# Optimization experiments

Hardware: AMD Instinct MI355X
Metric: run time of the kernel (lower is better)

Reference implementation:

```python
import jax, jax.numpy as jnp
import numpy as np

HEADS = 4
DIM_QK = 128
SCALE = DIM_QK ** (-0.5)


def rel_to_abs(x):
    # x: [B, Nh, L, 2L-1] -> [B, Nh, L, L] via the skew trick
    B, Nh, L, _ = x.shape
    x = jnp.pad(x, ((0, 0), (0, 0), (0, 0), (0, 1)))          # [B,Nh,L,2L]
    flat = x.reshape(B, Nh, L * 2 * L)
    flat = jnp.pad(flat, ((0, 0), (0, 0), (0, L - 1)))
    final = flat.reshape(B, Nh, L + 1, 2 * L - 1)
    return final[:, :, :L, L - 1:]


def relative_logits_1d(q, rel_k):
    # q: [B, Nh, H, W, d], rel_k: [2W-1, d] -> [B, Nh, H, H, W, W] (axes b h x i y j)
    B, Nh, H, W, _ = q.shape
    rl = jnp.einsum('bnhwd,md->bnhwm', q, rel_k)              # [B,Nh,H,W,2W-1]
    rl = rl.reshape(B, Nh * H, W, 2 * W - 1)
    rl = rel_to_abs(rl)                                        # [B,Nh*H,W,W]
    rl = rl.reshape(B, Nh, H, W, W)
    rl = jnp.broadcast_to(rl[:, :, :, None, :, :], (B, Nh, H, H, W, W))
    return rl


def rel_pos_logits(q, rel_height, rel_width, H, W):
    # q: [B, h, HW, d]
    B, h, L, d = q.shape
    qg = q.reshape(B, h, H, W, d)
    # width direction: b h x i y j -> b h (x y) (i j)
    rw = relative_logits_1d(qg, rel_width)                     # [B,h,H,H,W,W]
    rw = rw.transpose(0, 1, 2, 4, 3, 5).reshape(B, h, H * W, H * W)
    # height direction: transpose x<->y, then b h x i y j -> b h (y x) (j i)
    qh = qg.transpose(0, 1, 3, 2, 4)                           # [B,h,W,H,d]
    rh = relative_logits_1d(qh, rel_height)                    # [B,h,W,W,H,H]
    rh = rh.transpose(0, 1, 4, 2, 5, 3).reshape(B, h, H * W, H * W)
    return rw + rh


def setup_inputs() -> dict:
    key = jax.random.key(0)
    ks = jax.random.split(key, 5)
    B, C, H, W = 16, 512, 32, 32
    scale = DIM_QK ** (-0.5)
    return {
        'featuremap': jax.random.normal(ks[0], (B, C, H, W), jnp.float32),
        'w_qk': jax.random.normal(ks[1], (2 * HEADS * DIM_QK, C), jnp.float32) * (C ** -0.5),
        'w_v': jax.random.normal(ks[2], (HEADS * 128, C), jnp.float32) * (C ** -0.5),
        'rel_height': jax.random.normal(ks[3], (2 * H - 1, DIM_QK), jnp.float32) * scale,
        'rel_width': jax.random.normal(ks[4], (2 * W - 1, DIM_QK), jnp.float32) * scale,
    }


def reference(featuremap, w_qk, w_v, rel_height, rel_width):
    B, C, H, W = featuremap.shape
    L = H * W
    # 1x1 conv projections (no bias) == channel matmuls
    qk = jnp.einsum('bchw,oc->bohw', featuremap, w_qk)         # [B, 2*h*dqk, H, W]
    v = jnp.einsum('bchw,oc->bohw', featuremap, w_v)           # [B, h*dv, H, W]
    q, k = jnp.split(qk, 2, axis=1)

    def to_heads(x):
        # B (h d) H W -> B h (H W) d
        d = x.shape[1] // HEADS
        return x.reshape(B, HEADS, d, L).transpose(0, 1, 3, 2)

    q, k, v = to_heads(q), to_heads(k), to_heads(v)
    q = q * SCALE
    logits = jnp.einsum('bhxd,bhyd->bhxy', q, k)
    logits = logits + rel_pos_logits(q, rel_height, rel_width, H, W)
    weights = jax.nn.softmax(logits, axis=-1)
    attn_out = jnp.einsum('bhxy,bhyd->bhxd', weights, v)       # [B,h,L,dv]
    dv = attn_out.shape[-1]
    # B h (H W) d -> B (h d) H W
    return attn_out.transpose(0, 1, 3, 2).reshape(B, HEADS * dv, H, W)
```

## Files before the change

kernel.cpp:

```cpp
#include <hip/hip_runtime.h>
#include <stdint.h>

typedef __attribute__((ext_vector_type(4))) float f32x4;
typedef __attribute__((ext_vector_type(8))) short bf16x8;

#define DEV static __device__ __forceinline__

#define GLOAD16(g, l) __builtin_amdgcn_global_load_lds( \
    (const __attribute__((address_space(1))) void*)(g), \
    (__attribute__((address_space(3))) void*)(l), 16, 0, 0)

DEV unsigned short f2bf(float f){
  union { float f; uint32_t u; } v; v.f = f;
  return (unsigned short)((v.u + 0x7fffu + ((v.u >> 16) & 1u)) >> 16);
}

DEV uint32_t cvtpk(float a, float b){
  uint32_t r; asm("v_cvt_pk_bf16_f32 %0, %1, %2" : "=v"(r) : "v"(a), "v"(b)); return r;
}

DEV f32x4 mfma_bf16(bf16x8 a, bf16x8 b, f32x4 c){
  return __builtin_amdgcn_mfma_f32_16x16x32_bf16(a, b, c, 0, 0, 0);
}

__global__ __launch_bounds__(256) void k_transpose_cvt(const float* __restrict__ fm,
                                                       unsigned short* __restrict__ xt){
  __shared__ float tile[64][65];
  int b = blockIdx.z, c0 = blockIdx.y * 64, l0 = blockIdx.x * 64;
  int t = threadIdx.x;
  int lr = t >> 4;
  int lc4 = (t & 15) * 4;
  const float* src = fm + ((size_t)b * 512 + c0) * 1024 + l0;
  #pragma unroll
  for (int i = 0; i < 4; i++){
    int r = lr + i * 16;
    f32x4 v = *(const f32x4*)&src[(size_t)r * 1024 + lc4];
    tile[r][lc4] = v[0]; tile[r][lc4 + 1] = v[1];
    tile[r][lc4 + 2] = v[2]; tile[r][lc4 + 3] = v[3];
  }
  __syncthreads();
  int j = t & 7;
  int lrow = t >> 3;
  unsigned short* dst = xt + ((size_t)b * 1024 + l0) * 512 + c0;
  #pragma unroll
  for (int i = 0; i < 2; i++){
    int l = lrow + i * 32;
    unsigned short tmp[8];
    #pragma unroll
    for (int u = 0; u < 8; u++) tmp[u] = f2bf(tile[j * 8 + u][l]);
    *(uint4*)&dst[(size_t)l * 512 + j * 8] = *(const uint4*)tmp;
  }
}

__global__ __launch_bounds__(256) void k_wcvt(const float* __restrict__ wqk,
                                              const float* __restrict__ wv,
                                              unsigned short* __restrict__ wb){
  int idx = blockIdx.x * 256 + threadIdx.x;
  int e = idx * 4;
  if (e >= 1536 * 512) return;
  const float* src = (e < 1024 * 512) ? (wqk + e) : (wv + (e - 1024 * 512));
  f32x4 v = *(const f32x4*)src;
  unsigned short* d = wb + e;
  d[0] = f2bf(v[0]); d[1] = f2bf(v[1]); d[2] = f2bf(v[2]); d[3] = f2bf(v[3]);
}

template<int MODE>
__global__ __launch_bounds__(256, 3) void k_proj(const unsigned short* __restrict__ Abase,
                                                 const unsigned short* __restrict__ Bbase,
                                                 unsigned short* __restrict__ qbuf,
                                                 unsigned short* __restrict__ kbuf,
                                                 unsigned short* __restrict__ vbuf){
  __shared__ unsigned short Al[128][64];
  __shared__ unsigned short Bl[128][64];
  int b = blockIdx.z;
  const unsigned short* A = Abase + (MODE == 0 ? (size_t)b * 1024 * 512 : 0);
  const unsigned short* B = Bbase + (MODE == 0 ? 0 : (size_t)b * 1024 * 512);
  int m0 = blockIdx.x * 128, n0 = blockIdx.y * 128;
  int t = threadIdx.x;
  int lane = t & 63, w = t >> 6;
  int wm = (w >> 1) * 64, wn = (w & 1) * 64;
  int l15 = lane & 15, lg = lane >> 4;
  int srow = lane >> 3;
  int scol = (lane & 7) * 8;
  f32x4 acc[4][4];
  for (int m = 0; m < 4; m++) for (int n = 0; n < 4; n++) acc[m][n] = (f32x4)(0.f);
  for (int k0 = 0; k0 < 512; k0 += 64){
    __syncthreads();
    #pragma unroll
    for (int i = 0; i < 4; i++){
      int j = w * 4 + i;
      GLOAD16(&A[(size_t)(m0 + j * 8 + srow) * 512 + k0 + scol], &Al[j * 8][0]);
      GLOAD16(&B[(size_t)(n0 + j * 8 + srow) * 512 + k0 + scol], &Bl[j * 8][0]);
    }
    __syncthreads();
    for (int dc = 0; dc < 2; dc++){
      bf16x8 af[4], bfr[4];
      for (int m = 0; m < 4; m++) af[m]  = *(const bf16x8*)&Al[wm + m * 16 + l15][dc * 32 + lg * 8];
      for (int n = 0; n < 4; n++) bfr[n] = *(const bf16x8*)&Bl[wn + n * 16 + l15][dc * 32 + lg * 8];
      for (int m = 0; m < 4; m++)
        for (int n = 0; n < 4; n++)
          acc[m][n] = mfma_bf16(af[m], bfr[n], acc[m][n]);
    }
  }
  for (int m = 0; m < 4; m++) for (int n = 0; n < 4; n++) for (int r = 0; r < 4; r++){
    int row = m0 + wm + m * 16 + lg * 4 + r;
    int col = n0 + wn + n * 16 + l15;
    float val = acc[m][n][r];
    if (MODE == 0){
      if (col < 512){
        int h = col >> 7, d = col & 127;
        qbuf[(((size_t)b * 4 + h) * 1024 + row) * 128 + d] = f2bf(val * 0.08838834764831845f);
      } else {
        int c2 = col - 512;
        int h = c2 >> 7, d = c2 & 127;
        kbuf[(((size_t)b * 4 + h) * 1024 + row) * 128 + d] = f2bf(val);
      }
    } else {
      vbuf[(((size_t)b * 4 + (row >> 7)) * 128 + (row & 127)) * 1024 + col] = f2bf(val);
    }
  }
}

__global__ __launch_bounds__(64, 4) void k_rel(const unsigned short* __restrict__ qbuf,
                                               const float* __restrict__ relh,
                                               const float* __restrict__ relw,
                                               float* __restrict__ Rel){
  int xi = blockIdx.x;
  int bh = blockIdx.y;
  int mode = blockIdx.z;
  int lane = threadIdx.x;
  int l15 = lane & 15, lg = lane >> 4;
  const float* rel = (mode == 0) ? relh : relw;
  f32x4 acc[2][2];
  for (int m = 0; m < 2; m++) for (int n = 0; n < 2; n++) acc[m][n] = (f32x4)(0.f);
  for (int dc = 0; dc < 4; dc++){
    bf16x8 af[2], bb[2];
    for (int m = 0; m < 2; m++){
      int p = (mode == 0) ? (xi * 32 + m * 16 + l15) : ((m * 16 + l15) * 32 + xi);
      af[m] = *(const bf16x8*)&qbuf[((size_t)bh * 1024 + p) * 128 + dc * 32 + lg * 8];
    }
    for (int n = 0; n < 2; n++){
      int mrow = n * 16 + l15 - xi + 31;
      const float* rp = &rel[(size_t)mrow * 128 + dc * 32 + lg * 8];
      f32x4 r0 = *(const f32x4*)rp;
      f32x4 r1 = *(const f32x4*)(rp + 4);
      bf16x8 tt;
      for (int e = 0; e < 4; e++){ tt[e] = (short)f2bf(r0[e]); tt[e + 4] = (short)f2bf(r1[e]); }
      bb[n] = tt;
    }
    for (int m = 0; m < 2; m++)
      for (int n = 0; n < 2; n++)
        acc[m][n] = mfma_bf16(af[m], bb[n], acc[m][n]);
  }
  for (int m = 0; m < 2; m++) for (int n = 0; n < 2; n++) for (int r = 0; r < 4; r++){
    int a = m * 16 + lg * 4 + r;
    int outc = n * 16 + l15;
    int p = (mode == 0) ? (xi * 32 + a) : (a * 32 + xi);
    Rel[((size_t)bh * 1024 + p) * 64 + ((mode == 0) ? outc : 32 + outc)] = acc[m][n][r];
  }
}

__global__ __launch_bounds__(256, 2) void k_attn(const unsigned short* __restrict__ qbuf,
                                                 const unsigned short* __restrict__ kbuf,
                                                 const unsigned short* __restrict__ vbuf,
                                                 const float* __restrict__ Rel,
                                                 float* __restrict__ out){
  __shared__ unsigned short Kl[64 * 128];
  __shared__ unsigned short Vl[128 * 64];
  __shared__ unsigned short Pl[4][32 * 64];
  int bh = blockIdx.x;
  int q0 = blockIdx.y * 128;
  int t = threadIdx.x;
  int lane = t & 63, w = t >> 6;
  int l15 = lane & 15, lg = lane >> 4;
  int swz = (l15 & 7) * 8;
  int qw = q0 + w * 32;
  const unsigned short* qg = qbuf + (size_t)bh * 1024 * 128;
  const unsigned short* kg = kbuf + (size_t)bh * 1024 * 128;
  const unsigned short* vg = vbuf + (size_t)bh * 128 * 1024;
  const float* relbh = Rel + (size_t)bh * 1024 * 64;

  bf16x8 qf[2][4];
  #pragma unroll
  for (int cg = 0; cg < 2; cg++)
    #pragma unroll
    for (int dc = 0; dc < 4; dc++)
      qf[cg][dc] = *(const bf16x8*)&qg[(size_t)(qw + cg * 16 + l15) * 128 + dc * 32 + lg * 8];

  float rwv[2][2][4];
  #pragma unroll
  for (int cg = 0; cg < 2; cg++)
    #pragma unroll
    for (int kk = 0; kk < 2; kk++)
      #pragma unroll
      for (int r = 0; r < 4; r++)
        rwv[cg][kk][r] = relbh[(size_t)(qw + cg * 16 + l15) * 64 + 32 + kk * 16 + lg * 4 + r];

  bf16x8 ones;
  #pragma unroll
  for (int e = 0; e < 8; e++) ones[e] = (short)0x3F80;

  f32x4 o[8][2], osum[2];
  #pragma unroll
  for (int rg = 0; rg < 8; rg++) for (int cg = 0; cg < 2; cg++) o[rg][cg] = (f32x4)(0.f);
  osum[0] = (f32x4)(0.f); osum[1] = (f32x4)(0.f);

  bf16x8 kpre[4], vpre[4];
  #pragma unroll
  for (int i = 0; i < 4; i++){
    int c = t + i * 256;
    kpre[i] = *(const bf16x8*)&kg[(size_t)(c >> 4) * 128 + (c & 15) * 8];
    vpre[i] = *(const bf16x8*)&vg[(size_t)(c >> 3) * 1024 + (c & 7) * 8];
  }

  for (int kv0 = 0; kv0 < 1024; kv0 += 64){
    __syncthreads();
    #pragma unroll
    for (int i = 0; i < 4; i++){
      int c = t + i * 256;
      int kr = c >> 4;
      int vr = c >> 3;
      *(bf16x8*)&Kl[kr * 128 + (((c & 15) * 8) ^ ((kr & 7) * 8))] = kpre[i];
      *(bf16x8*)&Vl[vr * 64 + (((c & 7) * 8) ^ ((vr & 7) * 8))] = vpre[i];
    }
    __syncthreads();
    if (kv0 + 64 < 1024){
      int kvn = kv0 + 64;
      #pragma unroll
      for (int i = 0; i < 4; i++){
        int c = t + i * 256;
        kpre[i] = *(const bf16x8*)&kg[(size_t)(kvn + (c >> 4)) * 128 + (c & 15) * 8];
        vpre[i] = *(const bf16x8*)&vg[(size_t)(c >> 3) * 1024 + kvn + (c & 7) * 8];
      }
    }

    f32x4 s[4][2];
    #pragma unroll
    for (int g = 0; g < 4; g++) for (int cg = 0; cg < 2; cg++) s[g][cg] = (f32x4)(0.f);
    __builtin_amdgcn_s_setprio(1);
    #pragma unroll
    for (int dc = 0; dc < 4; dc++){
      bf16x8 kf[4];
      #pragma unroll
      for (int g = 0; g < 4; g++)
        kf[g] = *(const bf16x8*)&Kl[(g * 16 + l15) * 128 + ((dc * 32 + lg * 8) ^ swz)];
      #pragma unroll
      for (int g = 0; g < 4; g++)
        #pragma unroll
        for (int cg = 0; cg < 2; cg++)
          s[g][cg] = mfma_bf16(kf[g], qf[cg][dc], s[g][cg]);
    }
    __builtin_amdgcn_s_setprio(0);

    int y0 = kv0 >> 5;
    float rh[2][2];
    #pragma unroll
    for (int cg = 0; cg < 2; cg++){
      const float* rp = &relbh[(size_t)(qw + cg * 16 + l15) * 64];
      rh[cg][0] = rp[y0];
      rh[cg][1] = rp[y0 + 1];
    }

    #pragma unroll
    for (int h = 0; h < 2; h++){
      #pragma unroll
      for (int cg = 0; cg < 2; cg++){
        #pragma unroll
        for (int g = 0; g < 2; g++){
          int gi = h * 2 + g;
          float e0 = __expf(fminf(s[gi][cg][0] + rh[cg][h] + rwv[cg][g][0], 60.f));
          float e1 = __expf(fminf(s[gi][cg][1] + rh[cg][h] + rwv[cg][g][1], 60.f));
          float e2 = __expf(fminf(s[gi][cg][2] + rh[cg][h] + rwv[cg][g][2], 60.f));
          float e3 = __expf(fminf(s[gi][cg][3] + rh[cg][h] + rwv[cg][g][3], 60.f));
          uint2 pv = make_uint2(cvtpk(e0, e1), cvtpk(e2, e3));
          *(uint2*)&Pl[w][(cg * 16 + l15) * 64 + ((h * 32 + g * 16 + lg * 4) ^ swz)] = pv;
        }
      }
      __builtin_amdgcn_s_setprio(1);
      bf16x8 pf[2];
      #pragma unroll
      for (int cg = 0; cg < 2; cg++)
        pf[cg] = *(const bf16x8*)&Pl[w][(cg * 16 + l15) * 64 + ((h * 32 + lg * 8) ^ swz)];
      #pragma unroll
      for (int rg = 0; rg < 8; rg++){
        bf16x8 vf = *(const bf16x8*)&Vl[(rg * 16 + l15) * 64 + ((h * 32 + lg * 8) ^ swz)];
        #pragma unroll
        for (int cg = 0; cg < 2; cg++)
          o[rg][cg] = mfma_bf16(vf, pf[cg], o[rg][cg]);
      }
      #pragma unroll
      for (int cg = 0; cg < 2; cg++)
        osum[cg] = mfma_bf16(ones, pf[cg], osum[cg]);
      __builtin_amdgcn_s_setprio(0);
    }
  }
  float inv[2] = {1.f / osum[0][0], 1.f / osum[1][0]};
  float* outb = out + (size_t)bh * 128 * 1024;
  #pragma unroll
  for (int rg = 0; rg < 8; rg++)
    #pragma unroll
    for (int cg = 0; cg < 2; cg++)
      #pragma unroll
      for (int r = 0; r < 4; r++){
        int dv = rg * 16 + lg * 4 + r;
        int p = qw + cg * 16 + l15;
        outb[(size_t)dv * 1024 + p] = o[rg][cg][r] * inv[cg];
      }
}

extern "C" void kernel_launch(void* const* d_in, const int* in_sizes, int n_in,
                              void* d_out, int out_size, void* d_ws, size_t ws_size,
                              hipStream_t stream){
  const float* fm   = (const float*)d_in[0];
  const float* wqk  = (const float*)d_in[1];
  const float* wv   = (const float*)d_in[2];
  const float* relh = (const float*)d_in[3];
  const float* relw = (const float*)d_in[4];
  float* out = (float*)d_out;
  char* ws = (char*)d_ws;
  if (ws_size < (size_t)68681728) return;

  unsigned short* qb = (unsigned short*)(ws);
  unsigned short* kb = (unsigned short*)(ws + ((size_t)16 << 20));
  unsigned short* vb = (unsigned short*)(ws + ((size_t)32 << 20));
  unsigned short* xt = (unsigned short*)(ws + ((size_t)48 << 20));
  float* Rel         = (float*)(ws + ((size_t)48 << 20));
  unsigned short* wb = (unsigned short*)(ws + ((size_t)64 << 20));

  hipLaunchKernelGGL(k_transpose_cvt, dim3(16, 8, 16), dim3(256), 0, stream, fm, xt);
  hipLaunchKernelGGL(k_wcvt, dim3(768), dim3(256), 0, stream, wqk, wv, wb);
  hipLaunchKernelGGL(k_proj<0>, dim3(8, 8, 16), dim3(256), 0, stream, xt, wb, qb, kb, vb);
  hipLaunchKernelGGL(k_proj<1>, dim3(4, 8, 16), dim3(256), 0, stream,
                     wb + (size_t)1024 * 512, xt, qb, kb, vb);
  hipLaunchKernelGGL(k_rel, dim3(32, 64, 2), dim3(64), 0, stream, qb, relh, relw, Rel);
  hipLaunchKernelGGL(k_attn, dim3(64, 8), dim3(256), 0, stream, qb, kb, vb, Rel, out);
}
```

Measured before the change: 121.1 us.

## Read K/V fragments directly from global memory and widen k_rel blocks

```diff
diff --git a/kernel.cpp b/kernel.cpp
--- a/kernel.cpp
+++ b/kernel.cpp
@@ -121,14 +121,15 @@
   }
 }
 
-__global__ __launch_bounds__(64, 4) void k_rel(const unsigned short* __restrict__ qbuf,
-                                               const float* __restrict__ relh,
-                                               const float* __restrict__ relw,
-                                               float* __restrict__ Rel){
-  int xi = blockIdx.x;
+__global__ __launch_bounds__(256, 2) void k_rel(const unsigned short* __restrict__ qbuf,
+                                                const float* __restrict__ relh,
+                                                const float* __restrict__ relw,
+                                                float* __restrict__ Rel){
+  int t = threadIdx.x;
+  int lane = t & 63;
+  int xi = blockIdx.x * 4 + (t >> 6);
   int bh = blockIdx.y;
   int mode = blockIdx.z;
-  int lane = threadIdx.x;
   int l15 = lane & 15, lg = lane >> 4;
   const float* rel = (mode == 0) ? relh : relw;
   f32x4 acc[2][2];
@@ -165,8 +166,6 @@
                                                  const unsigned short* __restrict__ vbuf,
                                                  const float* __restrict__ Rel,
                                                  float* __restrict__ out){
-  __shared__ unsigned short Kl[64 * 128];
-  __shared__ unsigned short Vl[128 * 64];
   __shared__ unsigned short Pl[4][32 * 64];
   int bh = blockIdx.x;
   int q0 = blockIdx.y * 128;
@@ -205,52 +204,22 @@
   for (int rg = 0; rg < 8; rg++) for (int cg = 0; cg < 2; cg++) o[rg][cg] = (f32x4)(0.f);
   osum[0] = (f32x4)(0.f); osum[1] = (f32x4)(0.f);
 
-  bf16x8 kpre[4], vpre[4];
-  #pragma unroll
-  for (int i = 0; i < 4; i++){
-    int c = t + i * 256;
-    kpre[i] = *(const bf16x8*)&kg[(size_t)(c >> 4) * 128 + (c & 15) * 8];
-    vpre[i] = *(const bf16x8*)&vg[(size_t)(c >> 3) * 1024 + (c & 7) * 8];
-  }
-
   for (int kv0 = 0; kv0 < 1024; kv0 += 64){
-    __syncthreads();
-    #pragma unroll
-    for (int i = 0; i < 4; i++){
-      int c = t + i * 256;
-      int kr = c >> 4;
-      int vr = c >> 3;
-      *(bf16x8*)&Kl[kr * 128 + (((c & 15) * 8) ^ ((kr & 7) * 8))] = kpre[i];
-      *(bf16x8*)&Vl[vr * 64 + (((c & 7) * 8) ^ ((vr & 7) * 8))] = vpre[i];
-    }
-    __syncthreads();
-    if (kv0 + 64 < 1024){
-      int kvn = kv0 + 64;
-      #pragma unroll
-      for (int i = 0; i < 4; i++){
-        int c = t + i * 256;
-        kpre[i] = *(const bf16x8*)&kg[(size_t)(kvn + (c >> 4)) * 128 + (c & 15) * 8];
-        vpre[i] = *(const bf16x8*)&vg[(size_t)(c >> 3) * 1024 + kvn + (c & 7) * 8];
-      }
-    }
-
     f32x4 s[4][2];
     #pragma unroll
     for (int g = 0; g < 4; g++) for (int cg = 0; cg < 2; cg++) s[g][cg] = (f32x4)(0.f);
-    __builtin_amdgcn_s_setprio(1);
     #pragma unroll
     for (int dc = 0; dc < 4; dc++){
       bf16x8 kf[4];
       #pragma unroll
       for (int g = 0; g < 4; g++)
-        kf[g] = *(const bf16x8*)&Kl[(g * 16 + l15) * 128 + ((dc * 32 + lg * 8) ^ swz)];
+        kf[g] = *(const bf16x8*)&kg[(size_t)(kv0 + g * 16 + l15) * 128 + dc * 32 + lg * 8];
       #pragma unroll
       for (int g = 0; g < 4; g++)
         #pragma unroll
         for (int cg = 0; cg < 2; cg++)
           s[g][cg] = mfma_bf16(kf[g], qf[cg][dc], s[g][cg]);
     }
-    __builtin_amdgcn_s_setprio(0);
 
     int y0 = kv0 >> 5;
     float rh[2][2];
@@ -276,14 +245,13 @@
           *(uint2*)&Pl[w][(cg * 16 + l15) * 64 + ((h * 32 + g * 16 + lg * 4) ^ swz)] = pv;
         }
       }
-      __builtin_amdgcn_s_setprio(1);
       bf16x8 pf[2];
       #pragma unroll
       for (int cg = 0; cg < 2; cg++)
         pf[cg] = *(const bf16x8*)&Pl[w][(cg * 16 + l15) * 64 + ((h * 32 + lg * 8) ^ swz)];
       #pragma unroll
       for (int rg = 0; rg < 8; rg++){
-        bf16x8 vf = *(const bf16x8*)&Vl[(rg * 16 + l15) * 64 + ((h * 32 + lg * 8) ^ swz)];
+        bf16x8 vf = *(const bf16x8*)&vg[(size_t)(rg * 16 + l15) * 1024 + kv0 + h * 32 + lg * 8];
         #pragma unroll
         for (int cg = 0; cg < 2; cg++)
           o[rg][cg] = mfma_bf16(vf, pf[cg], o[rg][cg]);
@@ -291,7 +259,6 @@
       #pragma unroll
       for (int cg = 0; cg < 2; cg++)
         osum[cg] = mfma_bf16(ones, pf[cg], osum[cg]);
-      __builtin_amdgcn_s_setprio(0);
     }
   }
   float inv[2] = {1.f / osum[0][0], 1.f / osum[1][0]};
@@ -332,6 +299,6 @@
   hipLaunchKernelGGL(k_proj<0>, dim3(8, 8, 16), dim3(256), 0, stream, xt, wb, qb, kb, vb);
   hipLaunchKernelGGL(k_proj<1>, dim3(4, 8, 16), dim3(256), 0, stream,
                      wb + (size_t)1024 * 512, xt, qb, kb, vb);
-  hipLaunchKernelGGL(k_rel, dim3(32, 64, 2), dim3(64), 0, stream, qb, relh, relw, Rel);
+  hipLaunchKernelGGL(k_rel, dim3(8, 64, 2), dim3(256), 0, stream, qb, relh, relw, Rel);
   hipLaunchKernelGGL(k_attn, dim3(64, 8), dim3(256), 0, stream, qb, kb, vb, Rel, out);
 }
```

After: 212.2 us. 75.2% more time.

## Switch attention to 32x32x16 MFMA with register-resident P via permlane swap

Applied to the files above, without the earlier changes.

```diff
diff --git a/kernel.cpp b/kernel.cpp
--- a/kernel.cpp
+++ b/kernel.cpp
@@ -2,6 +2,7 @@
 #include <stdint.h>
 
 typedef __attribute__((ext_vector_type(4))) float f32x4;
+typedef __attribute__((ext_vector_type(16))) float f32x16;
 typedef __attribute__((ext_vector_type(8))) short bf16x8;
 
 #define DEV static __device__ __forceinline__
@@ -21,6 +22,10 @@
 
 DEV f32x4 mfma_bf16(bf16x8 a, bf16x8 b, f32x4 c){
   return __builtin_amdgcn_mfma_f32_16x16x32_bf16(a, b, c, 0, 0, 0);
+}
+
+DEV f32x16 mfma32(bf16x8 a, bf16x8 b, f32x16 c){
+  return __builtin_amdgcn_mfma_f32_32x32x16_bf16(a, b, c, 0, 0, 0);
 }
 
 __global__ __launch_bounds__(256) void k_transpose_cvt(const float* __restrict__ fm,
@@ -121,14 +126,15 @@
   }
 }
 
-__global__ __launch_bounds__(64, 4) void k_rel(const unsigned short* __restrict__ qbuf,
-                                               const float* __restrict__ relh,
-                                               const float* __restrict__ relw,
-                                               float* __restrict__ Rel){
-  int xi = blockIdx.x;
+__global__ __launch_bounds__(256, 2) void k_rel(const unsigned short* __restrict__ qbuf,
+                                                const float* __restrict__ relh,
+                                                const float* __restrict__ relw,
+                                                float* __restrict__ Rel){
+  int t = threadIdx.x;
+  int lane = t & 63;
+  int xi = blockIdx.x * 4 + (t >> 6);
   int bh = blockIdx.y;
   int mode = blockIdx.z;
-  int lane = threadIdx.x;
   int l15 = lane & 15, lg = lane >> 4;
   const float* rel = (mode == 0) ? relh : relw;
   f32x4 acc[2][2];
@@ -167,43 +173,36 @@
                                                  float* __restrict__ out){
   __shared__ unsigned short Kl[64 * 128];
   __shared__ unsigned short Vl[128 * 64];
-  __shared__ unsigned short Pl[4][32 * 64];
   int bh = blockIdx.x;
   int q0 = blockIdx.y * 128;
   int t = threadIdx.x;
   int lane = t & 63, w = t >> 6;
-  int l15 = lane & 15, lg = lane >> 4;
-  int swz = (l15 & 7) * 8;
-  int qw = q0 + w * 32;
+  int l31 = lane & 31, hi = lane >> 5;
+  int swz = (l31 & 7) * 8;
+  int q = q0 + w * 32 + l31;
   const unsigned short* qg = qbuf + (size_t)bh * 1024 * 128;
   const unsigned short* kg = kbuf + (size_t)bh * 1024 * 128;
   const unsigned short* vg = vbuf + (size_t)bh * 128 * 1024;
   const float* relbh = Rel + (size_t)bh * 1024 * 64;
 
-  bf16x8 qf[2][4];
-  #pragma unroll
-  for (int cg = 0; cg < 2; cg++)
-    #pragma unroll
-    for (int dc = 0; dc < 4; dc++)
-      qf[cg][dc] = *(const bf16x8*)&qg[(size_t)(qw + cg * 16 + l15) * 128 + dc * 32 + lg * 8];
-
-  float rwv[2][2][4];
-  #pragma unroll
-  for (int cg = 0; cg < 2; cg++)
-    #pragma unroll
-    for (int kk = 0; kk < 2; kk++)
-      #pragma unroll
-      for (int r = 0; r < 4; r++)
-        rwv[cg][kk][r] = relbh[(size_t)(qw + cg * 16 + l15) * 64 + 32 + kk * 16 + lg * 4 + r];
+  bf16x8 qf[8];
+  #pragma unroll
+  for (int ks = 0; ks < 8; ks++)
+    qf[ks] = *(const bf16x8*)&qg[(size_t)q * 128 + ks * 16 + hi * 8];
+
+  float rwv[16];
+  #pragma unroll
+  for (int r = 0; r < 16; r++)
+    rwv[r] = relbh[(size_t)q * 64 + 32 + (r & 3) + 8 * (r >> 2) + 4 * hi];
 
   bf16x8 ones;
   #pragma unroll
   for (int e = 0; e < 8; e++) ones[e] = (short)0x3F80;
 
-  f32x4 o[8][2], osum[2];
-  #pragma unroll
-  for (int rg = 0; rg < 8; rg++) for (int cg = 0; cg < 2; cg++) o[rg][cg] = (f32x4)(0.f);
-  osum[0] = (f32x4)(0.f); osum[1] = (f32x4)(0.f);
+  f32x16 o[4], osum;
+  #pragma unroll
+  for (int vb = 0; vb < 4; vb++) o[vb] = (f32x16)(0.f);
+  osum = (f32x16)(0.f);
 
   bf16x8 kpre[4], vpre[4];
   #pragma unroll
@@ -234,78 +233,60 @@
       }
     }
 
-    f32x4 s[4][2];
-    #pragma unroll
-    for (int g = 0; g < 4; g++) for (int cg = 0; cg < 2; cg++) s[g][cg] = (f32x4)(0.f);
+    f32x16 s0 = (f32x16)(0.f), s1 = (f32x16)(0.f);
     __builtin_amdgcn_s_setprio(1);
     #pragma unroll
-    for (int dc = 0; dc < 4; dc++){
-      bf16x8 kf[4];
+    for (int ks = 0; ks < 8; ks++){
+      bf16x8 kf0 = *(const bf16x8*)&Kl[(size_t)l31 * 128 + ((ks * 16 + hi * 8) ^ swz)];
+      bf16x8 kf1 = *(const bf16x8*)&Kl[(size_t)(32 + l31) * 128 + ((ks * 16 + hi * 8) ^ swz)];
+      s0 = mfma32(kf0, qf[ks], s0);
+      s1 = mfma32(kf1, qf[ks], s1);
+    }
+    __builtin_amdgcn_s_setprio(0);
+
+    float rh0 = relbh[(size_t)q * 64 + (kv0 >> 5)];
+    float rh1 = relbh[(size_t)q * 64 + (kv0 >> 5) + 1];
+
+    float pb0[16], pb1[16];
+    #pragma unroll
+    for (int r = 0; r < 16; r++){
+      pb0[r] = __expf(fminf(s0[r] + rh0 + rwv[r], 60.f));
+      pb1[r] = __expf(fminf(s1[r] + rh1 + rwv[r], 60.f));
+    }
+
+    __builtin_amdgcn_s_setprio(1);
+    #pragma unroll
+    for (int kk = 0; kk < 4; kk++){
+      const float* pb = (kk < 2) ? pb0 : pb1;
+      int kkk = kk & 1;
+      uint32_t c0 = cvtpk(pb[kkk * 8 + 0], pb[kkk * 8 + 1]);
+      uint32_t c1 = cvtpk(pb[kkk * 8 + 2], pb[kkk * 8 + 3]);
+      uint32_t c2 = cvtpk(pb[kkk * 8 + 4], pb[kkk * 8 + 5]);
+      uint32_t c3 = cvtpk(pb[kkk * 8 + 6], pb[kkk * 8 + 7]);
+      asm("v_permlane32_swap_b32 %0, %1" : "+v"(c0), "+v"(c2));
+      asm("v_permlane32_swap_b32 %0, %1" : "+v"(c1), "+v"(c3));
+      uint32_t words[4] = {c0, c1, c2, c3};
+      bf16x8 pfrag = *(const bf16x8*)words;
+      int vcol = kk * 16 + hi * 8;
       #pragma unroll
-      for (int g = 0; g < 4; g++)
-        kf[g] = *(const bf16x8*)&Kl[(g * 16 + l15) * 128 + ((dc * 32 + lg * 8) ^ swz)];
-      #pragma unroll
-      for (int g = 0; g < 4; g++)
-        #pragma unroll
-        for (int cg = 0; cg < 2; cg++)
-          s[g][cg] = mfma_bf16(kf[g], qf[cg][dc], s[g][cg]);
+      for (int vb = 0; vb < 4; vb++){
+        bf16x8 vf = *(const bf16x8*)&Vl[(size_t)(vb * 32 + l31) * 64 + (vcol ^ swz)];
+        o[vb] = mfma32(vf, pfrag, o[vb]);
+      }
+      osum = mfma32(ones, pfrag, osum);
     }
     __builtin_amdgcn_s_setprio(0);
-
-    int y0 = kv0 >> 5;
-    float rh[2][2];
-    #pragma unroll
-    for (int cg = 0; cg < 2; cg++){
-      const float* rp = &relbh[(size_t)(qw + cg * 16 + l15) * 64];
-      rh[cg][0] = rp[y0];
-      rh[cg][1] = rp[y0 + 1];
-    }
-
-    #pragma unroll
-    for (int h = 0; h < 2; h++){
-      #pragma unroll
-      for (int cg = 0; cg < 2; cg++){
-        #pragma unroll
-        for (int g = 0; g < 2; g++){
-          int gi = h * 2 + g;
-          float e0 = __expf(fminf(s[gi][cg][0] + rh[cg][h] + rwv[cg][g][0], 60.f));
-          float e1 = __expf(fminf(s[gi][cg][1] + rh[cg][h] + rwv[cg][g][1], 60.f));
-          float e2 = __expf(fminf(s[gi][cg][2] + rh[cg][h] + rwv[cg][g][2], 60.f));
-          float e3 = __expf(fminf(s[gi][cg][3] + rh[cg][h] + rwv[cg][g][3], 60.f));
-          uint2 pv = make_uint2(cvtpk(e0, e1), cvtpk(e2, e3));
-          *(uint2*)&Pl[w][(cg * 16 + l15) * 64 + ((h * 32 + g * 16 + lg * 4) ^ swz)] = pv;
-        }
-      }
-      __builtin_amdgcn_s_setprio(1);
-      bf16x8 pf[2];
-      #pragma unroll
-      for (int cg = 0; cg < 2; cg++)
-        pf[cg] = *(const bf16x8*)&Pl[w][(cg * 16 + l15) * 64 + ((h * 32 + lg * 8) ^ swz)];
-      #pragma unroll
-      for (int rg = 0; rg < 8; rg++){
-        bf16x8 vf = *(const bf16x8*)&Vl[(rg * 16 + l15) * 64 + ((h * 32 + lg * 8) ^ swz)];
-        #pragma unroll
-        for (int cg = 0; cg < 2; cg++)
-          o[rg][cg] = mfma_bf16(vf, pf[cg], o[rg][cg]);
-      }
-      #pragma unroll
-      for (int cg = 0; cg < 2; cg++)
-        osum[cg] = mfma_bf16(ones, pf[cg], osum[cg]);
-      __builtin_amdgcn_s_setprio(0);
-    }
-  }
-  float inv[2] = {1.f / osum[0][0], 1.f / osum[1][0]};
+  }
+
+  float inv = 1.f / osum[0];
   float* outb = out + (size_t)bh * 128 * 1024;
   #pragma unroll
-  for (int rg = 0; rg < 8; rg++)
-    #pragma unroll
-    for (int cg = 0; cg < 2; cg++)
-      #pragma unroll
-      for (int r = 0; r < 4; r++){
-        int dv = rg * 16 + lg * 4 + r;
-        int p = qw + cg * 16 + l15;
-        outb[(size_t)dv * 1024 + p] = o[rg][cg][r] * inv[cg];
-      }
+  for (int vb = 0; vb < 4; vb++)
+    #pragma unroll
+    for (int r = 0; r < 16; r++){
+      int dv = vb * 32 + (r & 3) + 8 * (r >> 2) + 4 * hi;
+      outb[(size_t)dv * 1024 + q] = o[vb][r] * inv;
+    }
 }
 
 extern "C" void kernel_launch(void* const* d_in, const int* in_sizes, int n_in,
@@ -332,6 +313,6 @@
   hipLaunchKernelGGL(k_proj<0>, dim3(8, 8, 16), dim3(256), 0, stream, xt, wb, qb, kb, vb);
   hipLaunchKernelGGL(k_proj<1>, dim3(4, 8, 16), dim3(256), 0, stream,
                      wb + (size_t)1024 * 512, xt, qb, kb, vb);
-  hipLaunchKernelGGL(k_rel, dim3(32, 64, 2), dim3(64), 0, stream, qb, relh, relw, Rel);
+  hipLaunchKernelGGL(k_rel, dim3(8, 64, 2), dim3(256), 0, stream, qb, relh, relw, Rel);
   hipLaunchKernelGGL(k_attn, dim3(64, 8), dim3(256), 0, stream, qb, kb, vb, Rel, out);
 }
```

Measured after the change: 119.6 us. About the same (-1.2%).
